# Optimization experiments

Measured on AMD Instinct MI355X. Metric: run time of the kernel, lower is better.

Reference implementation:

```python
import jax, jax.numpy as jnp
import numpy as np

F = 256          # in_features
T = 8            # num_fragment_ion_types = 4 types * 2 charges
N_MONO, N_CLEAV, N_FRAG, N_OUT = 150000, 100000, 80000, 40000
D_CLEAV, D_JOIN, D_COMB = 4, 2, 4


def setup_inputs() -> dict:
    key = jax.random.key(0)
    ks = jax.random.split(key, 14)
    s = 0.05
    return {
        "feature": jax.random.normal(ks[0], (N_MONO, F), jnp.float32),
        "Wg_lost": jax.random.normal(ks[1], (F, 1), jnp.float32) * s,
        "Wg_ret": jax.random.normal(ks[2], (F, 1), jnp.float32) * s,
        "W_ih": jax.random.normal(ks[3], (4 * F, 2 * F), jnp.float32) * s,
        "W_hh": jax.random.normal(ks[4], (4 * F, F), jnp.float32) * s,
        "b_ih": jax.random.normal(ks[5], (4 * F,), jnp.float32) * s,
        "b_hh": jax.random.normal(ks[6], (4 * F,), jnp.float32) * s,
        "Wg_frag": jax.random.normal(ks[7], (F, 1), jnp.float32) * s,
        "W_out": jax.random.normal(ks[8], (F, T), jnp.float32) * s,
        "b_out": jnp.zeros((T,), jnp.float32),
        "lost_src": jax.random.randint(ks[9], (N_CLEAV, D_CLEAV), 0, N_MONO),
        "retained_src": jax.random.randint(ks[10], (N_CLEAV, D_CLEAV), 0, N_MONO),
        "join_src": jax.random.randint(ks[11], (N_FRAG, D_JOIN), 0, N_CLEAV),
        "combine_src": jax.random.randint(ks[12], (N_OUT, D_COMB), 0, N_FRAG),
    }


def _attention_sum(h, Wg):
    # h: [N, D, F] mailbox; gate = Linear(F,1,no bias); softmax over neighbor axis
    logits = jnp.einsum('ndf,fo->ndo', h, Wg)          # [N, D, 1]
    a = jax.nn.softmax(logits, axis=1)
    return jnp.sum(a * h, axis=1)                       # [N, F]


def _lstm(x, W_ih, W_hh, b_ih, b_hh):
    # x: [N, L, I]; torch nn.LSTM gate order i,f,g,o; zero initial state
    N = x.shape[0]
    H = W_hh.shape[1]
    def step(carry, xt):
        h, c = carry
        gates = xt @ W_ih.T + h @ W_hh.T + b_ih + b_hh  # [N, 4H]
        i, f, g, o = jnp.split(gates, 4, axis=-1)
        c = jax.nn.sigmoid(f) * c + jax.nn.sigmoid(i) * jnp.tanh(g)
        h = jax.nn.sigmoid(o) * jnp.tanh(c)
        return (h, c), h
    init = (jnp.zeros((N, H), x.dtype), jnp.zeros((N, H), x.dtype))
    _, hs = jax.lax.scan(step, init, jnp.swapaxes(x, 0, 1))
    return jnp.swapaxes(hs, 0, 1)                       # [N, L, H]


def reference(feature, Wg_lost, Wg_ret, W_ih, W_hh, b_ih, b_hh,
              Wg_frag, W_out, b_out,
              lost_src, retained_src, join_src, combine_src):
    h_lost = _attention_sum(feature[lost_src], Wg_lost)        # [N_cleav, F]
    h_ret = _attention_sum(feature[retained_src], Wg_ret)      # [N_cleav, F]
    cleav = jnp.concatenate([h_lost, h_ret], axis=-1)          # [N_cleav, 2F]
    # Fragment pull over 'join' edges: LSTM over neighbor set, then attention sum
    hs = _lstm(cleav[join_src], W_ih, W_hh, b_ih, b_hh)        # [N_frag, D_join, F]
    frag = _attention_sum(hs, Wg_frag)                         # [N_frag, F]
    # Output head: Linear + ReLU
    frag_out = jax.nn.relu(frag @ W_out + b_out)               # [N_frag, T]
    # copy_u_sum over 'combine' edges: scatter-sum of src outputs to dst
    return frag_out[combine_src].sum(axis=1)                   # [N_out, T]
```

## Files before the change

kernel.cpp:

```cpp
#include <hip/hip_runtime.h>

typedef unsigned short u16;
typedef unsigned int u32;
typedef float f32x4 __attribute__((ext_vector_type(4)));
typedef __bf16 bf16x8 __attribute__((ext_vector_type(8)));

#define F 256
#define T_OUT 8
#define N_MONO 150000
#define N_CLEAV 100000
#define N_FRAG 80000
#define N_OUT 40000
#define M_CLEAV_PAD 100352

static __device__ __forceinline__ u16 f2bf(float f) {
  u32 u = __float_as_uint(f);
  u32 r = (u + 0x7FFFu + ((u >> 16) & 1u)) >> 16;
  return (u16)r;
}
static __device__ __forceinline__ float bf2f(u16 b) {
  return __uint_as_float(((u32)b) << 16);
}
static __device__ __forceinline__ float sigmoidf(float x) {
  return __frcp_rn(1.0f + __expf(-x));
}
static __device__ __forceinline__ float fast_tanh(float x) {
  return 1.0f - 2.0f * __frcp_rn(__expf(2.0f * x) + 1.0f);
}
static __device__ __forceinline__ void async_copy16(const u16* g, const u16* l) {
  __builtin_amdgcn_global_load_lds(
      (const __attribute__((address_space(1))) u32*)g,
      (__attribute__((address_space(3))) u32*)l,
      16, 0, 0);
}

__global__ __launch_bounds__(256) void prep_kernel(
    const float* __restrict__ Wih, const float* __restrict__ Whh,
    const float* __restrict__ bih, const float* __restrict__ bhh,
    u16* __restrict__ Wihb, u16* __restrict__ Whhb, float* __restrict__ bias) {
  int i = blockIdx.x * 256 + threadIdx.x;
  if (i < 1024 * 512) Wihb[i] = f2bf(Wih[i]);
  if (i < 1024 * 256) Whhb[i] = f2bf(Whh[i]);
  if (i < 1024) bias[i] = bih[i] + bhh[i];
}

__global__ __launch_bounds__(256) void attn_pull(
    const float* __restrict__ feat, const float* __restrict__ WgL,
    const float* __restrict__ WgR, const int* __restrict__ lostS,
    const int* __restrict__ retS, u16* __restrict__ cleav) {
  int wave = threadIdx.x >> 6, lane = threadIdx.x & 63;
  int n = blockIdx.x * 4 + wave;
  if (n >= N_CLEAV) return;
  const float4 wgl = *(const float4*)(WgL + lane * 4);
  const float4 wgr = *(const float4*)(WgR + lane * 4);
  for (int sg = 0; sg < 2; ++sg) {
    const int* src = sg ? retS : lostS;
    float4 wg = sg ? wgr : wgl;
    int4 ridx = *(const int4*)(src + n * 4);
    int r[4] = {ridx.x, ridx.y, ridx.z, ridx.w};
    float4 x[4];
#pragma unroll
    for (int d = 0; d < 4; ++d)
      x[d] = *(const float4*)(feat + (size_t)r[d] * F + lane * 4);
    float logit[4];
#pragma unroll
    for (int d = 0; d < 4; ++d) {
      float p = x[d].x * wg.x + x[d].y * wg.y + x[d].z * wg.z + x[d].w * wg.w;
#pragma unroll
      for (int off = 32; off; off >>= 1) p += __shfl_xor(p, off);
      logit[d] = p;
    }
    float mx = fmaxf(fmaxf(logit[0], logit[1]), fmaxf(logit[2], logit[3]));
    float e0 = __expf(logit[0] - mx), e1 = __expf(logit[1] - mx);
    float e2 = __expf(logit[2] - mx), e3 = __expf(logit[3] - mx);
    float inv = 1.f / (e0 + e1 + e2 + e3);
    float a0 = e0 * inv, a1 = e1 * inv, a2 = e2 * inv, a3 = e3 * inv;
    float4 acc;
    acc.x = a0 * x[0].x + a1 * x[1].x + a2 * x[2].x + a3 * x[3].x;
    acc.y = a0 * x[0].y + a1 * x[1].y + a2 * x[2].y + a3 * x[3].y;
    acc.z = a0 * x[0].z + a1 * x[1].z + a2 * x[2].z + a3 * x[3].z;
    acc.w = a0 * x[0].w + a1 * x[1].w + a2 * x[2].w + a3 * x[3].w;
    u32 lo = (u32)f2bf(acc.x) | ((u32)f2bf(acc.y) << 16);
    u32 hi = (u32)f2bf(acc.z) | ((u32)f2bf(acc.w) << 16);
    *(uint2*)(cleav + (size_t)n * 512 + sg * 256 + lane * 4) = make_uint2(lo, hi);
  }
}

template <int EPI, int K>
__global__ __launch_bounds__(256, 4) void gemm_bt(
    const u16* __restrict__ A, const u16* __restrict__ Bw,
    u16* __restrict__ C, const float* __restrict__ bias,
    int nper, int mstrips_valid) {
  __shared__ u16 As[3][128 * 32];
  __shared__ u16 Bs[3][128 * 32];
  const int flat = blockIdx.x;
  const int xcd = flat & 7;
  const int w = flat >> 3;
  const int mstrip = xcd * nper + (w >> 3);
  const int nstrip = w & 7;
  if (mstrip >= mstrips_valid) return;
  const int m0 = mstrip * 128;
  const int n0 = nstrip * 128;

  const int tid = threadIdx.x;
  const int lane = tid & 63;
  const int wave = tid >> 6;
  const int quad = lane >> 4;
  const int l16 = lane & 15;
  const int wm = (wave & 1) * 64;
  const int wn = (wave >> 1) * 64;

  f32x4 acc[4][4];
#pragma unroll
  for (int i = 0; i < 4; i++)
#pragma unroll
    for (int j = 0; j < 4; j++) acc[i][j] = (f32x4){0.f, 0.f, 0.f, 0.f};

  int srow[2], skoff[2], ldsoff[2];
#pragma unroll
  for (int jj = 0; jj < 2; jj++) {
    int c = jj * 256 + tid;
    srow[jj] = c >> 2;
    skoff[jj] = ((c & 3) ^ ((c >> 3) & 3)) * 8;
    ldsoff[jj] = (jj * 256 + (tid & ~63)) * 8;
  }
  const u16* Abase = A + (size_t)m0 * K;
  const u16* Bbase = Bw + (size_t)n0 * K;

  auto stage = [&](int buf, int k0) {
#pragma unroll
    for (int jj = 0; jj < 2; jj++)
      async_copy16(Abase + (size_t)srow[jj] * K + k0 + skoff[jj], &As[buf][ldsoff[jj]]);
#pragma unroll
    for (int jj = 0; jj < 2; jj++)
      async_copy16(Bbase + (size_t)srow[jj] * K + k0 + skoff[jj], &Bs[buf][ldsoff[jj]]);
  };

  constexpr int nK = K / 32;
  stage(0, 0);
  stage(1, 32);
#pragma unroll
  for (int t = 0; t < nK; ++t) {
    if (t < nK - 1) __builtin_amdgcn_s_waitcnt(0xF74);
    else            __builtin_amdgcn_s_waitcnt(0xF70);
    __builtin_amdgcn_s_barrier();
    if (t + 2 < nK) stage((t + 2) % 3, (t + 2) * 32);
    const int buf = t % 3;
    bf16x8 af[4], bfr[4];
#pragma unroll
    for (int i = 0; i < 4; i++) {
      int m = wm + i * 16 + l16;
      int jp = quad ^ ((m >> 1) & 3);
      af[i] = *(const bf16x8*)&As[buf][m * 32 + jp * 8];
    }
#pragma unroll
    for (int j = 0; j < 4; j++) {
      int n = wn + j * 16 + l16;
      int jp = quad ^ ((n >> 1) & 3);
      bfr[j] = *(const bf16x8*)&Bs[buf][n * 32 + jp * 8];
    }
#pragma unroll
    for (int i = 0; i < 4; i++)
#pragma unroll
      for (int j = 0; j < 4; j++)
        acc[i][j] = __builtin_amdgcn_mfma_f32_16x16x32_bf16(af[i], bfr[j], acc[i][j], 0, 0, 0);
  }

#pragma unroll
  for (int i = 0; i < 4; i++) {
    int mbase = m0 + wm + i * 16 + quad * 4;
#pragma unroll
    for (int j = 0; j < 4; j++) {
      int n = n0 + wn + j * 16 + l16;
      float badd = (EPI == 0) ? bias[n] : 0.f;
#pragma unroll
      for (int r = 0; r < 4; r++) {
        int m = mbase + r;
        C[(size_t)m * 1024 + n] = f2bf(acc[i][j][r] + badd);
      }
    }
  }
}

__global__ __launch_bounds__(256) void lstm_step1(
    const u16* __restrict__ P, const int* __restrict__ join,
    u16* __restrict__ h1, u16* __restrict__ c1) {
  int wave = threadIdx.x >> 6, lane = threadIdx.x & 63;
  int m = blockIdx.x * 4 + wave;
  if (m >= N_FRAG) return;
  int j0 = join[2 * m];
  const u16* row = P + (size_t)j0 * 1024 + lane * 4;
  ushort4 iv = *(const ushort4*)(row);
  ushort4 gv = *(const ushort4*)(row + 512);
  ushort4 ov = *(const ushort4*)(row + 768);
  const u16* ivp = (const u16*)&iv;
  const u16* gvp = (const u16*)&gv;
  const u16* ovp = (const u16*)&ov;
  ushort4 h4, c4;
  u16* h4p = (u16*)&h4;
  u16* c4p = (u16*)&c4;
#pragma unroll
  for (int k = 0; k < 4; k++) {
    float c = sigmoidf(bf2f(ivp[k])) * fast_tanh(bf2f(gvp[k]));
    float hv = sigmoidf(bf2f(ovp[k])) * fast_tanh(c);
    h4p[k] = f2bf(hv);
    c4p[k] = f2bf(c);
  }
  *(ushort4*)(h1 + (size_t)m * 256 + lane * 4) = h4;
  *(ushort4*)(c1 + (size_t)m * 256 + lane * 4) = c4;
}

__global__ __launch_bounds__(256) void lstm_step2_attn_out(
    const u16* __restrict__ G2, const u16* __restrict__ P,
    const int* __restrict__ join, const u16* __restrict__ c1,
    const u16* __restrict__ h1b, const float* __restrict__ Wg,
    const float* __restrict__ Wout, const float* __restrict__ bout,
    float* __restrict__ frag_out) {
  int wave = threadIdx.x >> 6, lane = threadIdx.x & 63;
  int m = blockIdx.x * 4 + wave;
  if (m >= N_FRAG) return;
  int j1 = join[2 * m + 1];
  const u16* row = G2 + (size_t)m * 1024 + lane * 4;
  const u16* prow = P + (size_t)j1 * 1024 + lane * 4;
  ushort4 iv = *(const ushort4*)(row);
  ushort4 fv = *(const ushort4*)(row + 256);
  ushort4 gv = *(const ushort4*)(row + 512);
  ushort4 ov = *(const ushort4*)(row + 768);
  ushort4 pi = *(const ushort4*)(prow);
  ushort4 pf = *(const ushort4*)(prow + 256);
  ushort4 pg = *(const ushort4*)(prow + 512);
  ushort4 po = *(const ushort4*)(prow + 768);
  ushort4 c4 = *(const ushort4*)(c1 + (size_t)m * 256 + lane * 4);
  ushort4 h4 = *(const ushort4*)(h1b + (size_t)m * 256 + lane * 4);
  float4 wg = *(const float4*)(Wg + lane * 4);
  const u16* ivp = (const u16*)&iv; const u16* pip = (const u16*)&pi;
  const u16* fvp = (const u16*)&fv; const u16* pfp = (const u16*)&pf;
  const u16* gvp = (const u16*)&gv; const u16* pgp = (const u16*)&pg;
  const u16* ovp = (const u16*)&ov; const u16* pop = (const u16*)&po;
  const u16* c4p = (const u16*)&c4;
  const u16* h4p = (const u16*)&h4;
  const float* wgp = (const float*)&wg;

  float h1v[4], h2v[4];
  float p1 = 0.f, p2 = 0.f;
#pragma unroll
  for (int k = 0; k < 4; k++) {
    float gi = bf2f(ivp[k]) + bf2f(pip[k]);
    float gf = bf2f(fvp[k]) + bf2f(pfp[k]);
    float gg = bf2f(gvp[k]) + bf2f(pgp[k]);
    float go = bf2f(ovp[k]) + bf2f(pop[k]);
    float c2 = sigmoidf(gf) * bf2f(c4p[k]) + sigmoidf(gi) * fast_tanh(gg);
    float h2 = sigmoidf(go) * fast_tanh(c2);
    h2v[k] = h2;
    h1v[k] = bf2f(h4p[k]);
    p1 += h1v[k] * wgp[k];
    p2 += h2 * wgp[k];
  }
#pragma unroll
  for (int off = 32; off; off >>= 1) {
    p1 += __shfl_xor(p1, off);
    p2 += __shfl_xor(p2, off);
  }
  float mx = fmaxf(p1, p2);
  float e1 = __expf(p1 - mx), e2 = __expf(p2 - mx);
  float inv = __frcp_rn(e1 + e2);
  float a1 = e1 * inv, a2 = e2 * inv;

  float acc[8];
#pragma unroll
  for (int t = 0; t < 8; t++) acc[t] = 0.f;
#pragma unroll
  for (int k = 0; k < 4; k++) {
    float frag = a1 * h1v[k] + a2 * h2v[k];
    int h = lane * 4 + k;
    float4 w0 = *(const float4*)(Wout + h * 8);
    float4 w1 = *(const float4*)(Wout + h * 8 + 4);
    acc[0] += frag * w0.x; acc[1] += frag * w0.y;
    acc[2] += frag * w0.z; acc[3] += frag * w0.w;
    acc[4] += frag * w1.x; acc[5] += frag * w1.y;
    acc[6] += frag * w1.z; acc[7] += frag * w1.w;
  }
#pragma unroll
  for (int off = 32; off; off >>= 1)
#pragma unroll
    for (int t = 0; t < 8; t++) acc[t] += __shfl_xor(acc[t], off);
  if (lane == 0) {
    float4 o0, o1;
    o0.x = fmaxf(acc[0] + bout[0], 0.f);
    o0.y = fmaxf(acc[1] + bout[1], 0.f);
    o0.z = fmaxf(acc[2] + bout[2], 0.f);
    o0.w = fmaxf(acc[3] + bout[3], 0.f);
    o1.x = fmaxf(acc[4] + bout[4], 0.f);
    o1.y = fmaxf(acc[5] + bout[5], 0.f);
    o1.z = fmaxf(acc[6] + bout[6], 0.f);
    o1.w = fmaxf(acc[7] + bout[7], 0.f);
    *(float4*)(frag_out + (size_t)m * 8) = o0;
    *(float4*)(frag_out + (size_t)m * 8 + 4) = o1;
  }
}

__global__ __launch_bounds__(256) void scatter_sum(
    const float* __restrict__ frag_out, const int* __restrict__ comb,
    float* __restrict__ out) {
  int tid = blockIdx.x * 256 + threadIdx.x;
  if (tid >= N_OUT * 8) return;
  int n = tid >> 3, t = tid & 7;
  float s = 0.f;
#pragma unroll
  for (int d = 0; d < 4; d++) {
    int f = comb[n * 4 + d];
    s += frag_out[(size_t)f * 8 + t];
  }
  out[tid] = s;
}

extern "C" void kernel_launch(void* const* d_in, const int* in_sizes, int n_in,
                              void* d_out, int out_size, void* d_ws, size_t ws_size,
                              hipStream_t stream) {
  const float* feature = (const float*)d_in[0];
  const float* WgL = (const float*)d_in[1];
  const float* WgR = (const float*)d_in[2];
  const float* Wih = (const float*)d_in[3];
  const float* Whh = (const float*)d_in[4];
  const float* bih = (const float*)d_in[5];
  const float* bhh = (const float*)d_in[6];
  const float* Wgf = (const float*)d_in[7];
  const float* Wout = (const float*)d_in[8];
  const float* bout = (const float*)d_in[9];
  const int* lostS = (const int*)d_in[10];
  const int* retS = (const int*)d_in[11];
  const int* joinS = (const int*)d_in[12];
  const int* combS = (const int*)d_in[13];
  float* out = (float*)d_out;

  char* ws = (char*)d_ws;
  size_t off = 0;
  auto alloc = [&](size_t bytes) -> char* {
    char* p = ws + off;
    off = (off + bytes + 255) & ~(size_t)255;
    return p;
  };
  u16* Wihb = (u16*)alloc((size_t)1024 * 512 * 2);
  u16* Whhb = (u16*)alloc((size_t)1024 * 256 * 2);
  float* bias = (float*)alloc(1024 * 4);
  u16* P = (u16*)alloc((size_t)M_CLEAV_PAD * 1024 * 2);
  u16* h1 = (u16*)alloc((size_t)N_FRAG * 256 * 2);
  u16* c1 = (u16*)alloc((size_t)N_FRAG * 256 * 2);
  float* frag_out = (float*)alloc((size_t)N_FRAG * 8 * 4);
  char* uni = alloc((size_t)M_CLEAV_PAD * 1024 * 2);
  u16* cleav = (u16*)uni;
  u16* gates2 = (u16*)uni;

  prep_kernel<<<2048, 256, 0, stream>>>(Wih, Whh, bih, bhh, Wihb, Whhb, bias);
  attn_pull<<<N_CLEAV / 4, 256, 0, stream>>>(feature, WgL, WgR, lostS, retS, cleav);
  gemm_bt<0, 512><<<784 * 8, 256, 0, stream>>>(cleav, Wihb, P, bias, 98, 784);
  lstm_step1<<<N_FRAG / 4, 256, 0, stream>>>(P, joinS, h1, c1);
  gemm_bt<1, 256><<<632 * 8, 256, 0, stream>>>(h1, Whhb, gates2, nullptr, 79, 625);
  lstm_step2_attn_out<<<N_FRAG / 4, 256, 0, stream>>>(
      gates2, P, joinS, c1, h1, Wgf, Wout, bout, frag_out);
  scatter_sum<<<(N_OUT * 8 + 255) / 256, 256, 0, stream>>>(frag_out, combS, out);
}
```

Baseline: 730.8 us.

## Replace 128x128 GEMM with 256x256 tile, 8-wave ping-pong pipelined kernel

Replaces the 128x128, 4-wave, triple-buffered bf16 GEMM with a 256x256 tile kernel that runs 8 waves per 512-thread block. K is staged in 64-wide chunks with double buffering, and each K-step is split into four MFMA phases, with async loads for the next step interleaved between barriers and s_setprio. The larger tile is meant to raise data reuse per LDS load and cut global traffic for both LSTM projection GEMMs. The cost is more registers and LDS per block, lower occupancy, and the second GEMM now computes padded rows past N_FRAG that read into neighbouring workspace.

```diff
diff --git a/kernel.cpp b/kernel.cpp
--- a/kernel.cpp
+++ b/kernel.cpp
@@ -87,97 +87,167 @@
 }
 
 template <int EPI, int K>
-__global__ __launch_bounds__(256, 4) void gemm_bt(
+__global__ __launch_bounds__(512, 2) void gemm256(
     const u16* __restrict__ A, const u16* __restrict__ Bw,
     u16* __restrict__ C, const float* __restrict__ bias,
     int nper, int mstrips_valid) {
-  __shared__ u16 As[3][128 * 32];
-  __shared__ u16 Bs[3][128 * 32];
+  __shared__ u16 sh[2][32768];
   const int flat = blockIdx.x;
   const int xcd = flat & 7;
   const int w = flat >> 3;
-  const int mstrip = xcd * nper + (w >> 3);
-  const int nstrip = w & 7;
+  const int mstrip = xcd * nper + (w >> 2);
+  const int nstrip = w & 3;
   if (mstrip >= mstrips_valid) return;
-  const int m0 = mstrip * 128;
-  const int n0 = nstrip * 128;
+  const int m0 = mstrip * 256;
+  const int n0 = nstrip * 256;
 
   const int tid = threadIdx.x;
   const int lane = tid & 63;
   const int wave = tid >> 6;
   const int quad = lane >> 4;
   const int l16 = lane & 15;
-  const int wm = (wave & 1) * 64;
-  const int wn = (wave >> 1) * 64;
-
-  f32x4 acc[4][4];
-#pragma unroll
-  for (int i = 0; i < 4; i++)
-#pragma unroll
-    for (int j = 0; j < 4; j++) acc[i][j] = (f32x4){0.f, 0.f, 0.f, 0.f};
-
-  int srow[2], skoff[2], ldsoff[2];
-#pragma unroll
-  for (int jj = 0; jj < 2; jj++) {
-    int c = jj * 256 + tid;
-    srow[jj] = c >> 2;
-    skoff[jj] = ((c & 3) ^ ((c >> 3) & 3)) * 8;
-    ldsoff[jj] = (jj * 256 + (tid & ~63)) * 8;
+  const int s7 = l16 & 7;
+  const int wm2 = wave >> 2;
+  const int wn4 = wave & 3;
+
+  const int arow = (wm2 * 128 + l16) * 64;
+  const int brow = 16384 + (wn4 * 64 + l16) * 64;
+  const int coff0 = ((0 + quad) ^ s7) * 8;
+  const int coff1 = ((4 + quad) ^ s7) * 8;
+
+  int srow[2], ssw[2], sdst[2];
+#pragma unroll
+  for (int j = 0; j < 2; j++) {
+    int c = j * 512 + tid;
+    int r = c >> 3, p = c & 7;
+    srow[j] = r;
+    ssw[j] = (p ^ (r & 7)) * 8;
+    sdst[j] = (j * 512 + (tid & ~63)) * 8;
   }
   const u16* Abase = A + (size_t)m0 * K;
   const u16* Bbase = Bw + (size_t)n0 * K;
 
-  auto stage = [&](int buf, int k0) {
-#pragma unroll
-    for (int jj = 0; jj < 2; jj++)
-      async_copy16(Abase + (size_t)srow[jj] * K + k0 + skoff[jj], &As[buf][ldsoff[jj]]);
-#pragma unroll
-    for (int jj = 0; jj < 2; jj++)
-      async_copy16(Bbase + (size_t)srow[jj] * K + k0 + skoff[jj], &Bs[buf][ldsoff[jj]]);
+  auto stage = [&](int buf, int mat, int h, int kt) {
+    const u16* gb = (mat ? Bbase : Abase) + (size_t)(h * 128) * K + kt * 64;
+    const u16* lb = &sh[buf][mat * 16384 + h * 8192];
+#pragma unroll
+    for (int j = 0; j < 2; j++)
+      async_copy16(gb + (size_t)srow[j] * K + ssw[j], lb + sdst[j]);
   };
 
-  constexpr int nK = K / 32;
-  stage(0, 0);
-  stage(1, 32);
+  f32x4 acc[8][4];
+#pragma unroll
+  for (int i = 0; i < 8; i++)
+#pragma unroll
+    for (int j = 0; j < 4; j++) acc[i][j] = (f32x4){0.f, 0.f, 0.f, 0.f};
+
+  constexpr int nK = K / 64;
+  stage(0, 0, 0, 0); stage(0, 0, 1, 0); stage(0, 1, 0, 0); stage(0, 1, 1, 0);
+  if (nK > 1) { stage(1, 1, 0, 1); stage(1, 1, 1, 1); }
+  __builtin_amdgcn_s_waitcnt(0xF74);
+  __builtin_amdgcn_s_barrier();
+
+  bf16x8 a[4][2], b0[2][2], b1[2][2];
 #pragma unroll
   for (int t = 0; t < nK; ++t) {
-    if (t < nK - 1) __builtin_amdgcn_s_waitcnt(0xF74);
+    const int bsel = t & 1;
+    const u16* S = &sh[bsel][0];
+
+#pragma unroll
+    for (int i = 0; i < 4; i++) {
+      a[i][0] = *(const bf16x8*)&S[arow + i * 1024 + coff0];
+      a[i][1] = *(const bf16x8*)&S[arow + i * 1024 + coff1];
+    }
+#pragma unroll
+    for (int j = 0; j < 2; j++) {
+      b0[j][0] = *(const bf16x8*)&S[brow + j * 1024 + coff0];
+      b0[j][1] = *(const bf16x8*)&S[brow + j * 1024 + coff1];
+    }
+    if (t + 1 < nK) stage(bsel ^ 1, 0, 0, t + 1);
+    __builtin_amdgcn_s_waitcnt(0xC87F);
+    __builtin_amdgcn_s_barrier();
+    __builtin_amdgcn_s_waitcnt(0xC07F);
+    __builtin_amdgcn_sched_barrier(0);
+    __builtin_amdgcn_s_setprio(1);
+#pragma unroll
+    for (int i = 0; i < 4; i++)
+#pragma unroll
+      for (int j = 0; j < 2; j++) {
+        acc[i][j] = __builtin_amdgcn_mfma_f32_16x16x32_bf16(a[i][0], b0[j][0], acc[i][j], 0, 0, 0);
+        acc[i][j] = __builtin_amdgcn_mfma_f32_16x16x32_bf16(a[i][1], b0[j][1], acc[i][j], 0, 0, 0);
+      }
+    __builtin_amdgcn_s_setprio(0);
+    __builtin_amdgcn_s_barrier();
+
+#pragma unroll
+    for (int j = 0; j < 2; j++) {
+      b1[j][0] = *(const bf16x8*)&S[brow + (2 + j) * 1024 + coff0];
+      b1[j][1] = *(const bf16x8*)&S[brow + (2 + j) * 1024 + coff1];
+    }
+    if (t + 1 < nK) stage(bsel ^ 1, 0, 1, t + 1);
+    __builtin_amdgcn_s_barrier();
+    __builtin_amdgcn_s_waitcnt(0xC07F);
+    __builtin_amdgcn_sched_barrier(0);
+    __builtin_amdgcn_s_setprio(1);
+#pragma unroll
+    for (int i = 0; i < 4; i++)
+#pragma unroll
+      for (int j = 0; j < 2; j++) {
+        acc[i][2 + j] = __builtin_amdgcn_mfma_f32_16x16x32_bf16(a[i][0], b1[j][0], acc[i][2 + j], 0, 0, 0);
+        acc[i][2 + j] = __builtin_amdgcn_mfma_f32_16x16x32_bf16(a[i][1], b1[j][1], acc[i][2 + j], 0, 0, 0);
+      }
+    __builtin_amdgcn_s_setprio(0);
+    __builtin_amdgcn_s_barrier();
+
+#pragma unroll
+    for (int i = 0; i < 4; i++) {
+      a[i][0] = *(const bf16x8*)&S[arow + (4 + i) * 1024 + coff0];
+      a[i][1] = *(const bf16x8*)&S[arow + (4 + i) * 1024 + coff1];
+    }
+    if (t + 2 < nK) stage(bsel, 1, 0, t + 2);
+    __builtin_amdgcn_s_barrier();
+    __builtin_amdgcn_s_waitcnt(0xC07F);
+    __builtin_amdgcn_sched_barrier(0);
+    __builtin_amdgcn_s_setprio(1);
+#pragma unroll
+    for (int i = 0; i < 4; i++)
+#pragma unroll
+      for (int j = 0; j < 2; j++) {
+        acc[4 + i][j] = __builtin_amdgcn_mfma_f32_16x16x32_bf16(a[i][0], b0[j][0], acc[4 + i][j], 0, 0, 0);
+        acc[4 + i][j] = __builtin_amdgcn_mfma_f32_16x16x32_bf16(a[i][1], b0[j][1], acc[4 + i][j], 0, 0, 0);
+      }
+    __builtin_amdgcn_s_setprio(0);
+    __builtin_amdgcn_s_barrier();
+
+    if (t + 2 < nK) stage(bsel, 1, 1, t + 2);
+    __builtin_amdgcn_s_barrier();
+    __builtin_amdgcn_s_setprio(1);
+#pragma unroll
+    for (int i = 0; i < 4; i++)
+#pragma unroll
+      for (int j = 0; j < 2; j++) {
+        acc[4 + i][2 + j] = __builtin_amdgcn_mfma_f32_16x16x32_bf16(a[i][0], b1[j][0], acc[4 + i][2 + j], 0, 0, 0);
+        acc[4 + i][2 + j] = __builtin_amdgcn_mfma_f32_16x16x32_bf16(a[i][1], b1[j][1], acc[4 + i][2 + j], 0, 0, 0);
+      }
+    __builtin_amdgcn_s_setprio(0);
+    if (t + 2 < nK) __builtin_amdgcn_s_waitcnt(0xF74);
     else            __builtin_amdgcn_s_waitcnt(0xF70);
     __builtin_amdgcn_s_barrier();
-    if (t + 2 < nK) stage((t + 2) % 3, (t + 2) * 32);
-    const int buf = t % 3;
-    bf16x8 af[4], bfr[4];
-#pragma unroll
-    for (int i = 0; i < 4; i++) {
-      int m = wm + i * 16 + l16;
-      int jp = quad ^ ((m >> 1) & 3);
-      af[i] = *(const bf16x8*)&As[buf][m * 32 + jp * 8];
-    }
+  }
+
+  float badd[4];
+#pragma unroll
+  for (int j = 0; j < 4; j++)
+    badd[j] = (EPI == 0) ? bias[n0 + wn4 * 64 + j * 16 + l16] : 0.f;
+#pragma unroll
+  for (int i = 0; i < 8; i++) {
+    const int mrow = m0 + wm2 * 128 + i * 16 + quad * 4;
 #pragma unroll
     for (int j = 0; j < 4; j++) {
-      int n = wn + j * 16 + l16;
-      int jp = quad ^ ((n >> 1) & 3);
-      bfr[j] = *(const bf16x8*)&Bs[buf][n * 32 + jp * 8];
-    }
-#pragma unroll
-    for (int i = 0; i < 4; i++)
-#pragma unroll
-      for (int j = 0; j < 4; j++)
-        acc[i][j] = __builtin_amdgcn_mfma_f32_16x16x32_bf16(af[i], bfr[j], acc[i][j], 0, 0, 0);
-  }
-
-#pragma unroll
-  for (int i = 0; i < 4; i++) {
-    int mbase = m0 + wm + i * 16 + quad * 4;
-#pragma unroll
-    for (int j = 0; j < 4; j++) {
-      int n = n0 + wn + j * 16 + l16;
-      float badd = (EPI == 0) ? bias[n] : 0.f;
-#pragma unroll
-      for (int r = 0; r < 4; r++) {
-        int m = mbase + r;
-        C[(size_t)m * 1024 + n] = f2bf(acc[i][j][r] + badd);
-      }
+      const int n = n0 + wn4 * 64 + j * 16 + l16;
+#pragma unroll
+      for (int r = 0; r < 4; r++)
+        C[(size_t)(mrow + r) * 1024 + n] = f2bf(acc[i][j][r] + badd[j]);
     }
   }
 }
@@ -353,9 +423,9 @@
 
   prep_kernel<<<2048, 256, 0, stream>>>(Wih, Whh, bih, bhh, Wihb, Whhb, bias);
   attn_pull<<<N_CLEAV / 4, 256, 0, stream>>>(feature, WgL, WgR, lostS, retS, cleav);
-  gemm_bt<0, 512><<<784 * 8, 256, 0, stream>>>(cleav, Wihb, P, bias, 98, 784);
+  gemm256<0, 512><<<1568, 512, 0, stream>>>(cleav, Wihb, P, bias, 49, 392);
   lstm_step1<<<N_FRAG / 4, 256, 0, stream>>>(P, joinS, h1, c1);
-  gemm_bt<1, 256><<<632 * 8, 256, 0, stream>>>(h1, Whhb, gates2, nullptr, 79, 625);
+  gemm256<1, 256><<<1280, 512, 0, stream>>>(h1, Whhb, gates2, nullptr, 40, 313);
   lstm_step2_attn_out<<<N_FRAG / 4, 256, 0, stream>>>(
       gates2, P, joinS, c1, h1, Wgf, Wout, bout, frag_out);
   scatter_sum<<<(N_OUT * 8 + 255) / 256, 256, 0, stream>>>(frag_out, combS, out);
```

Result: faster. 683.5 us (-6.5%).
